# Performance work log

Hardware: AMD Instinct MI355X
Metric: run time of the kernel (lower is better)

## Reference

```python
import jax, jax.numpy as jnp
import numpy as np

N, E, F_IN, G, C = 100000, 3200000, 64, 1024, 10
BN_EPS = 1e-5


def _glorot(key, shape):
    fan_in, fan_out = shape[0], shape[1]
    lim = jnp.sqrt(6.0 / (fan_in + fan_out))
    return jax.random.uniform(key, shape, jnp.float32, -lim, lim)


def setup_inputs() -> dict:
    key = jax.random.key(0)
    ks = jax.random.split(key, 20)
    x = jax.random.normal(ks[0], (N, F_IN), jnp.float32)
    edge_index = jax.random.randint(ks[1], (2, E), 0, N, jnp.int64)
    batch = jnp.sort(jax.random.randint(ks[2], (N,), 0, G, jnp.int64))
    p = {
        'W1a': _glorot(ks[3], (F_IN, 128)), 'b1a': jnp.zeros((128,), jnp.float32),
        'W1b': _glorot(ks[4], (128, 128)), 'b1b': jnp.zeros((128,), jnp.float32),
        'g1': jnp.ones((128,), jnp.float32), 'be1': jnp.zeros((128,), jnp.float32),
        'W2a': _glorot(ks[5], (128, 64)), 'b2a': jnp.zeros((64,), jnp.float32),
        'W2b': _glorot(ks[6], (64, 64)), 'b2b': jnp.zeros((64,), jnp.float32),
        'g2': jnp.ones((64,), jnp.float32), 'be2': jnp.zeros((64,), jnp.float32),
        'W3a': _glorot(ks[7], (64, 32)), 'b3a': jnp.zeros((32,), jnp.float32),
        'W3b': _glorot(ks[8], (32, 32)), 'b3b': jnp.zeros((32,), jnp.float32),
        'g3': jnp.ones((32,), jnp.float32), 'be3': jnp.zeros((32,), jnp.float32),
        'Wf1': _glorot(ks[9], (32, 128)), 'bf1': jnp.zeros((128,), jnp.float32),
        'Wf2': _glorot(ks[10], (128, 64)), 'bf2': jnp.zeros((64,), jnp.float32),
        'Wf3': _glorot(ks[11], (64, C)), 'bf3': jnp.zeros((C,), jnp.float32),
    }
    return {'x': x, 'edge_index': edge_index, 'batch': batch, **p}


def _gin(x, src, dst, Wa, ba, Wb, bb):
    # GINConv (eps=0): h = MLP(x + sum_{j->i} x_j)
    agg = jax.ops.segment_sum(x[src], dst, num_segments=N)
    h = jax.nn.relu((x + agg) @ Wa + ba)
    return h @ Wb + bb


def _bn(x, g, b):
    # BatchNorm1d, training-mode batch statistics (biased variance)
    mu = jnp.mean(x, axis=0)
    var = jnp.mean((x - mu) ** 2, axis=0)
    return (x - mu) * jax.lax.rsqrt(var + BN_EPS) * g + b


def reference(x, edge_index, batch,
              W1a, b1a, W1b, b1b, g1, be1,
              W2a, b2a, W2b, b2b, g2, be2,
              W3a, b3a, W3b, b3b, g3, be3,
              Wf1, bf1, Wf2, bf2, Wf3, bf3):
    src, dst = edge_index[0], edge_index[1]
    z = _bn(jax.nn.relu(_gin(x, src, dst, W1a, b1a, W1b, b1b)), g1, be1)
    z = _bn(jax.nn.relu(_gin(z, src, dst, W2a, b2a, W2b, b2b)), g2, be2)
    z = _bn(jax.nn.relu(_gin(z, src, dst, W3a, b3a, W3b, b3b)), g3, be3)
    # global_add_pool over graph ids
    z = jax.ops.segment_sum(z, batch, num_segments=G)  # [G, 32]
    cr = jax.nn.relu(z @ Wf1 + bf1)
    cr = jax.nn.relu(cr @ Wf2 + bf2)  # dropout = identity (eval)
    cr = cr @ Wf3 + bf3
    return cr.reshape(-1, C)
```

## Files before the change

### kernel.cpp

```cpp
#include <hip/hip_runtime.h>

#define BN_EPS 1e-5f

typedef _Float16 f16;
typedef _Float16 f16x8 __attribute__((ext_vector_type(8)));
typedef _Float16 f16x4 __attribute__((ext_vector_type(4)));
typedef float f32x4 __attribute__((ext_vector_type(4)));

#define NBLK 512
#define BSHIFT 8
#define BMASK 255

__device__ __forceinline__ void wfrag_one(const float* __restrict__ W, f16* __restrict__ out,
        int FIN, int FOUT, int f,
        const float* __restrict__ stats, int NC, const float* __restrict__ g, float invN) {
    int j = f & 7;
    int lane = (f >> 3) & 63;
    int tile = f >> 9;
    int NT = FOUT >> 4;
    int t = tile % NT, s = tile / NT;
    int k = s * 32 + (lane >> 4) * 8 + j;
    int n = t * 16 + (lane & 15);
    float w = W[(size_t)k * FOUT + n];
    if (stats) {
        float s1 = 0.0f, s2 = 0.0f;
        for (int c = 0; c < NC; c++) {
            s1 += stats[c * 2 * FIN + k];
            s2 += stats[c * 2 * FIN + FIN + k];
        }
        float mu = s1 * invN;
        float var = fmaxf(s2 * invN - mu * mu, 0.0f);
        w *= rsqrtf(var + BN_EPS) * g[k];
    }
    out[f] = (f16)w;
}

__global__ __launch_bounds__(256) void setup_count(const float4* __restrict__ x,
        f16x4* __restrict__ xh, int n4,
        const float* __restrict__ W1a, f16* __restrict__ Wh1a,
        const float* __restrict__ W1b, f16* __restrict__ Wh1b,
        const float* __restrict__ W2b, f16* __restrict__ Wh2b,
        const float* __restrict__ W3b, f16* __restrict__ Wh3b,
        const int* __restrict__ dst, int* __restrict__ hist,
        int NBK, int CHUNK, int E) {
    __shared__ int lh[512];
    const int BC = (n4 + 255) / 256;
    int bid = blockIdx.x;
    const int t = threadIdx.x;
    if (bid < BC) {
        int i = bid * 256 + t;
        if (i < n4) {
            float4 v = x[i];
            f16x4 o;
            o.x = (f16)v.x; o.y = (f16)v.y; o.z = (f16)v.z; o.w = (f16)v.w;
            xh[i] = o;
        }
        return;
    }
    bid -= BC;
    if (bid < 116) {
        if (bid < 32)       wfrag_one(W1a, Wh1a, 64, 128, bid * 256 + t, nullptr, 1, nullptr, 0.f);
        else if (bid < 96)  wfrag_one(W1b, Wh1b, 128, 128, (bid - 32) * 256 + t, nullptr, 1, nullptr, 0.f);
        else if (bid < 112) wfrag_one(W2b, Wh2b, 64, 64, (bid - 96) * 256 + t, nullptr, 1, nullptr, 0.f);
        else                wfrag_one(W3b, Wh3b, 32, 32, (bid - 112) * 256 + t, nullptr, 1, nullptr, 0.f);
        return;
    }
    const int blk = bid - 116;
    for (int r = t; r < 512; r += 256) lh[r] = 0;
    __syncthreads();
    const int e0 = blk * CHUNK, e1 = min(E, e0 + CHUNK);
    const int nq = (e1 - e0) >> 2;
    const int4* d4 = (const int4*)(dst + e0);
    for (int q = t; q < nq; q += 256) {
        int4 v = d4[q];
        atomicAdd(&lh[v.x >> BSHIFT], 1);
        atomicAdd(&lh[v.y >> BSHIFT], 1);
        atomicAdd(&lh[v.z >> BSHIFT], 1);
        atomicAdd(&lh[v.w >> BSHIFT], 1);
    }
    for (int e = e0 + (nq << 2) + t; e < e1; e += 256) atomicAdd(&lh[dst[e] >> BSHIFT], 1);
    __syncthreads();
    for (int r = t; r < NBK; r += 256) hist[r * NBLK + blk] = lh[r];
}

__global__ __launch_bounds__(512) void bkt_bscan(int* __restrict__ hist,
        int* __restrict__ btot) {
    __shared__ int sh[512];
    const int b = blockIdx.x, t = threadIdx.x;
    int v = hist[b * NBLK + t];
    sh[t] = v;
    __syncthreads();
    for (int d = 1; d < 512; d <<= 1) {
        int u = (t >= d) ? sh[t - d] : 0;
        __syncthreads();
        sh[t] += u;
        __syncthreads();
    }
    hist[b * NBLK + t] = sh[t] - v;
    if (t == 511) btot[b] = sh[511];
}

__global__ __launch_bounds__(512) void bkt_scatter(const int* __restrict__ src,
        const int* __restrict__ dst, const int* __restrict__ hist,
        const int* __restrict__ btot, int* __restrict__ bucketed,
        int NBK, int CHUNK, int E) {
    __shared__ int sc[512];
    __shared__ int lc[512];
    const int blk = blockIdx.x, t = threadIdx.x;
    int v = (t < NBK) ? btot[t] : 0;
    sc[t] = v;
    __syncthreads();
    for (int d = 1; d < 512; d <<= 1) {
        int u = (t >= d) ? sc[t - d] : 0;
        __syncthreads();
        sc[t] += u;
        __syncthreads();
    }
    if (t < NBK) lc[t] = (sc[t] - v) + hist[t * NBLK + blk];
    __syncthreads();
    const int e0 = blk * CHUNK, e1 = min(E, e0 + CHUNK);
    const int nq = (e1 - e0) >> 2;
    const int4* d4 = (const int4*)(dst + e0);
    const int4* s4 = (const int4*)(src + e0);
    for (int q = t; q < nq; q += 512) {
        int4 d = d4[q];
        int4 s = s4[q];
        int sl;
        sl = atomicAdd(&lc[d.x >> BSHIFT], 1); bucketed[sl] = ((d.x & BMASK) << 18) | s.x;
        sl = atomicAdd(&lc[d.y >> BSHIFT], 1); bucketed[sl] = ((d.y & BMASK) << 18) | s.y;
        sl = atomicAdd(&lc[d.z >> BSHIFT], 1); bucketed[sl] = ((d.z & BMASK) << 18) | s.z;
        sl = atomicAdd(&lc[d.w >> BSHIFT], 1); bucketed[sl] = ((d.w & BMASK) << 18) | s.w;
    }
    for (int e = e0 + (nq << 2) + t; e < e1; e += 512) {
        int d = dst[e];
        int slot = atomicAdd(&lc[d >> BSHIFT], 1);
        bucketed[slot] = ((d & BMASK) << 18) | src[e];
    }
}

__global__ __launch_bounds__(512) void bkt_csr(const int* __restrict__ bucketed,
        const int* __restrict__ btot, int* __restrict__ off,
        int* __restrict__ elist, int NBK, int N, int E) {
    __shared__ int sc[512];
    __shared__ int lh[256];
    __shared__ int lc[256];
    __shared__ int sh[256];
    const int b = blockIdx.x, t = threadIdx.x;
    int v = (t < NBK) ? btot[t] : 0;
    sc[t] = v;
    __syncthreads();
    for (int d = 1; d < 512; d <<= 1) {
        int u = (t >= d) ? sc[t - d] : 0;
        __syncthreads();
        sc[t] += u;
        __syncthreads();
    }
    const int cnt  = btot[b];
    const int base = sc[b] - cnt;
    if (b == 0 && t == 0) off[N] = E;
    const int b0 = b << BSHIFT;
    const int R = min(N - b0, 256);
    if (t < 256) lh[t] = 0;
    __syncthreads();
    for (int i = t; i < cnt; i += 512) atomicAdd(&lh[bucketed[base + i] >> 18], 1);
    __syncthreads();
    int v0 = 0;
    if (t < 256) { v0 = lh[t]; sh[t] = v0; }
    __syncthreads();
    for (int d = 1; d < 256; d <<= 1) {
        int u = 0;
        if (t < 256 && t >= d) u = sh[t - d];
        __syncthreads();
        if (t < 256) sh[t] += u;
        __syncthreads();
    }
    if (t < 256) { int ex = sh[t] - v0; lh[t] = ex; lc[t] = ex; }
    __syncthreads();
    if (t < R) off[b0 + t] = base + lh[t];
    for (int i = t; i < cnt; i += 512) {
        int p = bucketed[base + i];
        int rk = atomicAdd(&lc[p >> 18], 1);
        elist[base + rk] = p & 0x3FFFF;
    }
}

template<int F, int FOUT, bool STATS, bool AFFINE, typename OutT>
__global__ __launch_bounds__(256) void gather_gemm(const int* __restrict__ off,
        const int* __restrict__ elist, const f16* __restrict__ in,
        const f16* __restrict__ Wf, const float* __restrict__ bias,
        const float* __restrict__ av, const float* __restrict__ ab,
        OutT* __restrict__ Out, float* __restrict__ stats, int N) {
    constexpr int TPN = F / 8;
    constexpr int NPB = 256 / TPN;
    constexpr int SPB = NPB / 16;
    constexpr int WPS = 4 / SPB;
    constexpr int NTF = FOUT / 16;
    constexpr int NTW = NTF / WPS;
    constexpr int NS = F / 32;
    constexpr int LDW = F + 8;
    __shared__ f16 Hl[NPB * LDW];
    __shared__ float Ss[STATS ? 2 * FOUT : 1];
    if (STATS) for (int z = threadIdx.x; z < 2 * FOUT; z += 256) Ss[z] = 0.0f;

    const int base = blockIdx.x * NPB;
    const int rl = threadIdx.x / TPN;
    const int i = base + rl;
    const int l = threadIdx.x & (TPN - 1);
    if (i < N) {
        const int j0 = l * 8;
        const f16x8* __restrict__ inv = (const f16x8*)in;
        f16x8 s = inv[(size_t)i * TPN + l];
        float a[8];
#pragma unroll
        for (int u = 0; u < 8; u++) a[u] = (float)s[u];
        int k = off[i], e = off[i + 1];
        const float cnt = (float)(e - k + 1);
        if (k + 6 <= e) {
            f16x8 c0 = inv[(size_t)elist[k + 0] * TPN + l];
            f16x8 c1 = inv[(size_t)elist[k + 1] * TPN + l];
            f16x8 c2 = inv[(size_t)elist[k + 2] * TPN + l];
            f16x8 c3 = inv[(size_t)elist[k + 3] * TPN + l];
            f16x8 c4 = inv[(size_t)elist[k + 4] * TPN + l];
            f16x8 c5 = inv[(size_t)elist[k + 5] * TPN + l];
            k += 6;
            for (; k + 6 <= e; k += 6) {
                f16x8 d0 = inv[(size_t)elist[k + 0] * TPN + l];
                f16x8 d1 = inv[(size_t)elist[k + 1] * TPN + l];
                f16x8 d2 = inv[(size_t)elist[k + 2] * TPN + l];
                f16x8 d3 = inv[(size_t)elist[k + 3] * TPN + l];
                f16x8 d4 = inv[(size_t)elist[k + 4] * TPN + l];
                f16x8 d5 = inv[(size_t)elist[k + 5] * TPN + l];
#pragma unroll
                for (int u = 0; u < 8; u++)
                    a[u] += (((float)c0[u] + (float)c1[u]) + ((float)c2[u] + (float)c3[u]))
                          + ((float)c4[u] + (float)c5[u]);
                c0 = d0; c1 = d1; c2 = d2; c3 = d3; c4 = d4; c5 = d5;
            }
#pragma unroll
            for (int u = 0; u < 8; u++)
                a[u] += (((float)c0[u] + (float)c1[u]) + ((float)c2[u] + (float)c3[u]))
                      + ((float)c4[u] + (float)c5[u]);
        }
        if (k + 4 <= e) {
            f16x8 c0 = inv[(size_t)elist[k + 0] * TPN + l];
            f16x8 c1 = inv[(size_t)elist[k + 1] * TPN + l];
            f16x8 c2 = inv[(size_t)elist[k + 2] * TPN + l];
            f16x8 c3 = inv[(size_t)elist[k + 3] * TPN + l];
            k += 4;
#pragma unroll
            for (int u = 0; u < 8; u++)
                a[u] += ((float)c0[u] + (float)c1[u]) + ((float)c2[u] + (float)c3[u]);
        }
        for (; k < e; k++) {
            f16x8 p = inv[(size_t)elist[k] * TPN + l];
#pragma unroll
            for (int u = 0; u < 8; u++) a[u] += (float)p[u];
        }
        if (AFFINE) {
            float4 vv0 = *(const float4*)(av + j0);
            float4 vv1 = *(const float4*)(av + j0 + 4);
            float4 bb0 = *(const float4*)(ab + j0);
            float4 bb1 = *(const float4*)(ab + j0 + 4);
            a[0] = fmaxf(fmaf(cnt, vv0.x, a[0] + bb0.x), 0.0f);
            a[1] = fmaxf(fmaf(cnt, vv0.y, a[1] + bb0.y), 0.0f);
            a[2] = fmaxf(fmaf(cnt, vv0.z, a[2] + bb0.z), 0.0f);
            a[3] = fmaxf(fmaf(cnt, vv0.w, a[3] + bb0.w), 0.0f);
            a[4] = fmaxf(fmaf(cnt, vv1.x, a[4] + bb1.x), 0.0f);
            a[5] = fmaxf(fmaf(cnt, vv1.y, a[5] + bb1.y), 0.0f);
            a[6] = fmaxf(fmaf(cnt, vv1.z, a[6] + bb1.z), 0.0f);
            a[7] = fmaxf(fmaf(cnt, vv1.w, a[7] + bb1.w), 0.0f);
        }
        f16x8 o;
#pragma unroll
        for (int u = 0; u < 8; u++) o[u] = (f16)a[u];
        *(f16x8*)&Hl[rl * LDW + j0] = o;
    }
    __syncthreads();

    const int wid = threadIdx.x >> 6;
    const int lane = threadIdx.x & 63;
    const int col = lane & 15;
    const int quad = lane >> 4;
    const int sid = wid / WPS;
    const int cg = wid % WPS;
    const int m0 = base + sid * 16;
    if (m0 < N) {
        f16x8 Bf[NS][NTW];
#pragma unroll
        for (int s = 0; s < NS; s++)
#pragma unroll
            for (int t = 0; t < NTW; t++)
                Bf[s][t] = *(const f16x8*)&Wf[((s * NTF + cg * NTW + t) << 9) + (lane << 3)];
        f32x4 acc[NTW];
#pragma unroll
        for (int t = 0; t < NTW; t++) {
            float b = bias[(cg * NTW + t) * 16 + col];
            acc[t] = (f32x4){b, b, b, b};
        }
        f16x8 Af[NS];
        const int rbase = (sid * 16 + col) * LDW + quad * 8;
#pragma unroll
        for (int s = 0; s < NS; s++) Af[s] = *(const f16x8*)&Hl[rbase + s * 32];
#pragma unroll
        for (int t = 0; t < NTW; t++)
#pragma unroll
            for (int s = 0; s < NS; s++)
                acc[t] = __builtin_amdgcn_mfma_f32_16x16x32_f16(Af[s], Bf[s][t], acc[t], 0, 0, 0);
#pragma unroll
        for (int t = 0; t < NTW; t++) {
            float v0 = fmaxf(acc[t][0], 0.0f);
            float v1 = fmaxf(acc[t][1], 0.0f);
            float v2 = fmaxf(acc[t][2], 0.0f);
            float v3 = fmaxf(acc[t][3], 0.0f);
            OutT* o = Out + (size_t)(m0 + quad * 4) * FOUT + (cg * NTW + t) * 16 + col;
            o[0]        = (OutT)v0;
            o[FOUT]     = (OutT)v1;
            o[2 * FOUT] = (OutT)v2;
            o[3 * FOUT] = (OutT)v3;
            if (STATS) {
                float s1 = (v0 + v1) + (v2 + v3);
                float s2 = (v0 * v0 + v1 * v1) + (v2 * v2 + v3 * v3);
                s1 += __shfl_xor(s1, 16); s1 += __shfl_xor(s1, 32);
                s2 += __shfl_xor(s2, 16); s2 += __shfl_xor(s2, 32);
                if (quad == 0) {
                    atomicAdd(&Ss[(cg * NTW + t) * 16 + col], s1);
                    atomicAdd(&Ss[FOUT + (cg * NTW + t) * 16 + col], s2);
                }
            }
        }
    }
    if (STATS) {
        __syncthreads();
        float* stc = stats + (blockIdx.x & 7) * 2 * FOUT;
        for (int z = threadIdx.x; z < 2 * FOUT; z += 256) atomicAdd(&stc[z], Ss[z]);
    }
}

__global__ __launch_bounds__(256) void layerprep_kernel(const float* __restrict__ W,
        f16* __restrict__ Wh, int FIN, int FOUT,
        const float* __restrict__ stats, int NC, const float* __restrict__ g,
        const float* __restrict__ be, float* __restrict__ v, float invN) {
    if (blockIdx.x == 0) {
        __shared__ float sh_s[128];
        const int t = threadIdx.x;
        if (t < FIN) {
            float s1 = 0.0f, s2 = 0.0f;
            for (int c = 0; c < NC; c++) {
                s1 += stats[c * 2 * FIN + t];
                s2 += stats[c * 2 * FIN + FIN + t];
            }
            float mu = s1 * invN;
            float var = fmaxf(s2 * invN - mu * mu, 0.0f);
            float sc = rsqrtf(var + BN_EPS) * g[t];
            sh_s[t] = be[t] - mu * sc;
        }
        __syncthreads();
        for (int j = t; j < FOUT; j += 256) {
            float acc = 0.0f;
            for (int k = 0; k < FIN; k++)
                acc = fmaf(sh_s[k], W[(size_t)k * FOUT + j], acc);
            v[j] = acc;
        }
        return;
    }
    int f = (blockIdx.x - 1) * 256 + threadIdx.x;
    if (f < FIN * FOUT) wfrag_one(W, Wh, FIN, FOUT, f, stats, NC, g, invN);
}

template<int FIN, int FOUT, int CT, bool STATS, bool RELU, bool BIAS, typename OutT>
__global__ __launch_bounds__(256) void gemm_mfma(const f16* __restrict__ A,
        const f16* __restrict__ Wf, const float* __restrict__ bias,
        OutT* __restrict__ Out, float* __restrict__ stats, int N) {
    constexpr int NS = FIN / 32;
    constexpr int NTF = FOUT / 16;
    constexpr int NT = CT / 16;
    constexpr int NCB = FOUT / CT;
    __shared__ float Ss[STATS ? 2 * FOUT : 1];
    if (STATS) {
        for (int i = threadIdx.x; i < 2 * FOUT; i += 256) Ss[i] = 0.0f;
        __syncthreads();
    }
    const int rb = blockIdx.x;
    const int RB = gridDim.x;
    const int wid = threadIdx.x >> 6;
    const int lane = threadIdx.x & 63;
    const int col = lane & 15;
    const int quad = lane >> 4;

    float bj[NCB][NT];
#pragma unroll
    for (int cb = 0; cb < NCB; cb++)
#pragma unroll
        for (int t = 0; t < NT; t++)
            bj[cb][t] = BIAS ? bias[(cb * NT + t) * 16 + col] : 0.0f;

    float ls[NCB][NT], ls2[NCB][NT];
#pragma unroll
    for (int cb = 0; cb < NCB; cb++)
#pragma unroll
        for (int t = 0; t < NT; t++) { ls[cb][t] = 0.0f; ls2[cb][t] = 0.0f; }

    const int S = N >> 4;
    for (int sidx = rb * 4 + wid; sidx < S; sidx += RB * 4) {
        const int m0 = sidx << 4;
        const f16* a0 = A + (size_t)(m0 + col) * FIN + (quad << 3);
        f16x8 Af[NS];
#pragma unroll
        for (int s = 0; s < NS; s++) Af[s] = *(const f16x8*)(a0 + s * 32);
#pragma unroll
        for (int cb = 0; cb < NCB; cb++) {
            const int t0 = cb * NT;
            f16x8 Bf[NS][NT];
#pragma unroll
            for (int s = 0; s < NS; s++)
#pragma unroll
                for (int t = 0; t < NT; t++)
                    Bf[s][t] = *(const f16x8*)&Wf[((s * NTF + t0 + t) << 9) + (lane << 3)];
            f32x4 acc[NT];
#pragma unroll
            for (int t = 0; t < NT; t++) acc[t] = (f32x4){bj[cb][t], bj[cb][t], bj[cb][t], bj[cb][t]};
#pragma unroll
            for (int t = 0; t < NT; t++)
#pragma unroll
                for (int s = 0; s < NS; s++)
                    acc[t] = __builtin_amdgcn_mfma_f32_16x16x32_f16(Af[s], Bf[s][t], acc[t], 0, 0, 0);
#pragma unroll
            for (int t = 0; t < NT; t++) {
                float v0 = acc[t][0], v1 = acc[t][1], v2 = acc[t][2], v3 = acc[t][3];
                if (RELU) {
                    v0 = fmaxf(v0, 0.0f); v1 = fmaxf(v1, 0.0f);
                    v2 = fmaxf(v2, 0.0f); v3 = fmaxf(v3, 0.0f);
                }
                if (STATS) {
                    ls[cb][t]  += (v0 + v1) + (v2 + v3);
                    ls2[cb][t] += (v0 * v0 + v1 * v1) + (v2 * v2 + v3 * v3);
                }
                OutT* o = Out + (size_t)(m0 + quad * 4) * FOUT + (t0 + t) * 16 + col;
                o[0]        = (OutT)v0;
                o[FOUT]     = (OutT)v1;
                o[2 * FOUT] = (OutT)v2;
                o[3 * FOUT] = (OutT)v3;
            }
        }
    }

    if (STATS) {
#pragma unroll
        for (int cb = 0; cb < NCB; cb++)
#pragma unroll
            for (int t = 0; t < NT; t++) {
                float s1 = ls[cb][t], s2 = ls2[cb][t];
                s1 += __shfl_xor(s1, 16); s1 += __shfl_xor(s1, 32);
                s2 += __shfl_xor(s2, 16); s2 += __shfl_xor(s2, 32);
                if (quad == 0) {
                    atomicAdd(&Ss[(cb * NT + t) * 16 + col], s1);
                    atomicAdd(&Ss[FOUT + (cb * NT + t) * 16 + col], s2);
                }
            }
        __syncthreads();
        float* stc = stats + (blockIdx.x & 7) * 2 * FOUT;
        for (int i = threadIdx.x; i < 2 * FOUT; i += 256) atomicAdd(&stc[i], Ss[i]);
    }
}

__global__ __launch_bounds__(256) void bn_pool_kernel(const float* __restrict__ y,
        const float* __restrict__ stats, int NC, const float* __restrict__ gw,
        const float* __restrict__ bw, const int* __restrict__ batch,
        float* __restrict__ pool, int N, float invN) {
    constexpr int F = 32, CH = 64;
    int q = threadIdx.x >> 5;
    int j = threadIdx.x & 31;
    int r0 = (blockIdx.x * 8 + q) * CH;
    if (r0 >= N) return;
    int r1 = min(r0 + CH, N);
    float s1 = 0.0f, s2 = 0.0f;
    for (int c = 0; c < NC; c++) {
        s1 += stats[c * 2 * F + j];
        s2 += stats[c * 2 * F + F + j];
    }
    float mu = s1 * invN;
    float var = fmaxf(s2 * invN - mu * mu, 0.0f);
    float sc = rsqrtf(var + BN_EPS) * gw[j];
    float sh = bw[j] - mu * sc;
    int curg = batch[r0];
    float acc = 0.0f;
    for (int r = r0; r < r1; r++) {
        int g = batch[r];
        if (g != curg) {
            atomicAdd(pool + (size_t)curg * 32 + j, acc);
            acc = 0.0f;
            curg = g;
        }
        acc = fmaf(y[(size_t)r * 32 + j], sc, sh + acc);
    }
    atomicAdd(pool + (size_t)curg * 32 + j, acc);
}

__global__ __launch_bounds__(128) void fc_kernel(const float* __restrict__ pool,
        const float* __restrict__ Wf1, const float* __restrict__ bf1,
        const float* __restrict__ Wf2, const float* __restrict__ bf2,
        const float* __restrict__ Wf3, const float* __restrict__ bf3,
        float* __restrict__ out) {
    __shared__ float zin[32];
    __shared__ float h1[128];
    __shared__ float h2[64];
    const int gidx = blockIdx.x;
    const int t = threadIdx.x;
    if (t < 32) zin[t] = pool[(size_t)gidx * 32 + t];
    __syncthreads();
    {
        float a = bf1[t];
        for (int k = 0; k < 32; k++) a = fmaf(zin[k], Wf1[k * 128 + t], a);
        h1[t] = fmaxf(a, 0.0f);
    }
    __syncthreads();
    if (t < 64) {
        float a = bf2[t];
        for (int k = 0; k < 128; k++) a = fmaf(h1[k], Wf2[k * 64 + t], a);
        h2[t] = fmaxf(a, 0.0f);
    }
    __syncthreads();
    if (t < 10) {
        float a = bf3[t];
        for (int k = 0; k < 64; k++) a = fmaf(h2[k], Wf3[k * 10 + t], a);
        out[(size_t)gidx * 10 + t] = a;
    }
}

extern "C" void kernel_launch(void* const* d_in, const int* in_sizes, int n_in,
                              void* d_out, int out_size, void* d_ws, size_t ws_size,
                              hipStream_t stream) {
    const float* x   = (const float*)d_in[0];
    const int*  ei   = (const int*)d_in[1];
    const int*  batch= (const int*)d_in[2];
    const float* W1a = (const float*)d_in[3];  const float* b1a = (const float*)d_in[4];
    const float* W1b = (const float*)d_in[5];  const float* b1b = (const float*)d_in[6];
    const float* g1  = (const float*)d_in[7];  const float* be1 = (const float*)d_in[8];
    const float* W2a = (const float*)d_in[9];  const float* b2a = (const float*)d_in[10];
    const float* W2b = (const float*)d_in[11]; const float* b2b = (const float*)d_in[12];
    const float* g2  = (const float*)d_in[13]; const float* be2 = (const float*)d_in[14];
    const float* W3a = (const float*)d_in[15]; const float* b3a = (const float*)d_in[16];
    const float* W3b = (const float*)d_in[17]; const float* b3b = (const float*)d_in[18];
    const float* g3  = (const float*)d_in[19]; const float* be3 = (const float*)d_in[20];
    const float* Wf1 = (const float*)d_in[21]; const float* bf1 = (const float*)d_in[22];
    const float* Wf2 = (const float*)d_in[23]; const float* bf2 = (const float*)d_in[24];
    const float* Wf3 = (const float*)d_in[25]; const float* bf3 = (const float*)d_in[26];

    const int N = in_sizes[2];
    const int E = in_sizes[1] / 2;
    const int G = out_size / 10;
    const int* src = ei;
    const int* dst = ei + E;

    const int NBK = (N + BMASK) >> BSHIFT;
    const int CHUNK = (((E + NBLK - 1) / NBLK) + 3) & ~3;

    float* B0   = (float*)d_ws;
    float* B1   = B0 + (size_t)N * 128;
    float* pool = B1 + (size_t)N * 128;
    float* st1  = pool + (size_t)G * 32;
    float* st2c = st1 + 2048;
    float* st3c = st2c + 1024;
    int* off    = (int*)(st3c + 512);
    int* elist  = off + (N + 1);
    float* v2   = (float*)(elist + E);
    float* v3   = v2 + 64;
    int* btot   = (int*)(v3 + 32);
    f16* Wh1a   = (f16*)(btot + NBK);
    f16* Wh1b   = Wh1a + 64 * 128;
    f16* Wh2a   = Wh1b + 128 * 128;
    f16* Wh2b   = Wh2a + 128 * 64;
    f16* Wh3a   = Wh2b + 64 * 64;
    f16* Wh3b   = Wh3a + 64 * 32;

    int* bucketed = (int*)B1;
    int* hist     = bucketed + E;

    f16* xh    = (f16*)B0;
    f16* H1    = (f16*)B0 + (size_t)N * 64;
    f16* Y1    = (f16*)B1 + (size_t)N * 64;
    f16* Z1    = (f16*)B0;
    f16* Y2    = (f16*)B0 + (size_t)N * 64;
    f16* Z2    = (f16*)B0;
    float* Y3  = B1 + (size_t)N * 64;

    hipMemsetAsync(pool, 0, ((size_t)G * 32 + 2048 + 1024 + 512) * sizeof(float), stream);

    const float invN = 1.0f / (float)N;
    const int GG = 640;

    {
        int BC = (N * 16 + 255) / 256;
        setup_count<<<BC + 116 + NBLK, 256, 0, stream>>>(
            (const float4*)x, (f16x4*)xh, N * 16,
            W1a, Wh1a, W1b, Wh1b, W2b, Wh2b, W3b, Wh3b,
            dst, hist, NBK, CHUNK, E);
    }

    bkt_bscan  <<<NBK, 512, 0, stream>>>(hist, btot);
    bkt_scatter<<<NBLK, 512, 0, stream>>>(src, dst, hist, btot, bucketed, NBK, CHUNK, E);
    bkt_csr    <<<NBK, 512, 0, stream>>>(bucketed, btot, off, elist, NBK, N, E);

    gather_gemm<64, 128, false, false, f16><<<(N + 31) / 32, 256, 0, stream>>>(
        off, elist, xh, Wh1a, b1a, nullptr, nullptr, H1, nullptr, N);
    gemm_mfma<128, 128, 64, true, true, true, f16><<<GG, 256, 0, stream>>>(H1, Wh1b, b1b, Y1, st1, N);

    layerprep_kernel<<<33, 256, 0, stream>>>(W2a, Wh2a, 128, 64, st1, 8, g1, be1, v2, invN);
    gemm_mfma<128, 64, 64, false, false, false, f16><<<GG, 256, 0, stream>>>(Y1, Wh2a, nullptr, Z1, nullptr, N);
    gather_gemm<64, 64, true, true, f16><<<(N + 31) / 32, 256, 0, stream>>>(
        off, elist, Z1, Wh2b, b2b, v2, b2a, Y2, st2c, N);

    layerprep_kernel<<<9, 256, 0, stream>>>(W3a, Wh3a, 64, 32, st2c, 8, g2, be2, v3, invN);
    gemm_mfma<64, 32, 32, false, false, false, f16><<<GG, 256, 0, stream>>>(Y2, Wh3a, nullptr, Z2, nullptr, N);
    gather_gemm<32, 32, true, true, float><<<(N + 63) / 64, 256, 0, stream>>>(
        off, elist, Z2, Wh3b, b3b, v3, b3a, Y3, st3c, N);

    bn_pool_kernel<<<(N + 511) / 512, 256, 0, stream>>>(Y3, st3c, 8, g3, be3, batch, pool, N, invN);

    fc_kernel<<<G, 128, 0, stream>>>(pool, Wf1, bf1, Wf2, bf2, Wf3, bf3, (float*)d_out);
}
```

Baseline: 459.9 us.

## Store features in column-slab layout and split gather from GEMM

Feature matrices now sit in a sliced layout, with 8-column f16 slabs stored contiguously per slab (slab-major, node-minor), and the GEMM kernels read and write that layout. The fused gather+GEMM kernel is split into a slice-parallel gather kernel plus a separate MFMA GEMM launch. Each gather block handles one 8-column slab, so a slab's random neighbor reads hit a smaller working set and may cache better in L2. The cost is an extra kernel launch per layer and a full round trip of the aggregated features through global memory.

```diff
diff --git a/kernel.cpp b/kernel.cpp
--- a/kernel.cpp
+++ b/kernel.cpp
@@ -4,7 +4,6 @@
 
 typedef _Float16 f16;
 typedef _Float16 f16x8 __attribute__((ext_vector_type(8)));
-typedef _Float16 f16x4 __attribute__((ext_vector_type(4)));
 typedef float f32x4 __attribute__((ext_vector_type(4)));
 
 #define NBLK 512
@@ -36,7 +35,7 @@
 }
 
 __global__ __launch_bounds__(256) void setup_count(const float4* __restrict__ x,
-        f16x4* __restrict__ xh, int n4,
+        f16* __restrict__ xh, int N,
         const float* __restrict__ W1a, f16* __restrict__ Wh1a,
         const float* __restrict__ W1b, f16* __restrict__ Wh1b,
         const float* __restrict__ W2b, f16* __restrict__ Wh2b,
@@ -44,16 +43,20 @@
         const int* __restrict__ dst, int* __restrict__ hist,
         int NBK, int CHUNK, int E) {
     __shared__ int lh[512];
-    const int BC = (n4 + 255) / 256;
+    const int BC = (N + 31) / 32;
     int bid = blockIdx.x;
     const int t = threadIdx.x;
     if (bid < BC) {
-        int i = bid * 256 + t;
-        if (i < n4) {
-            float4 v = x[i];
-            f16x4 o;
-            o.x = (f16)v.x; o.y = (f16)v.y; o.z = (f16)v.z; o.w = (f16)v.w;
-            xh[i] = o;
+        int r = t >> 3, sl = t & 7;
+        int i = bid * 32 + r;
+        if (i < N) {
+            const float4* xr = x + (size_t)i * 16 + sl * 2;
+            float4 v0 = xr[0];
+            float4 v1 = xr[1];
+            f16x8 o;
+            o[0] = (f16)v0.x; o[1] = (f16)v0.y; o[2] = (f16)v0.z; o[3] = (f16)v0.w;
+            o[4] = (f16)v1.x; o[5] = (f16)v1.y; o[6] = (f16)v1.z; o[7] = (f16)v1.w;
+            ((f16x8*)xh)[(size_t)sl * N + i] = o;
         }
         return;
     }
@@ -184,156 +187,65 @@
     }
 }
 
-template<int F, int FOUT, bool STATS, bool AFFINE, typename OutT>
-__global__ __launch_bounds__(256) void gather_gemm(const int* __restrict__ off,
+template<int F, bool AFFINE>
+__global__ __launch_bounds__(256) void gather_slice(const int* __restrict__ off,
         const int* __restrict__ elist, const f16* __restrict__ in,
-        const f16* __restrict__ Wf, const float* __restrict__ bias,
         const float* __restrict__ av, const float* __restrict__ ab,
-        OutT* __restrict__ Out, float* __restrict__ stats, int N) {
-    constexpr int TPN = F / 8;
-    constexpr int NPB = 256 / TPN;
-    constexpr int SPB = NPB / 16;
-    constexpr int WPS = 4 / SPB;
-    constexpr int NTF = FOUT / 16;
-    constexpr int NTW = NTF / WPS;
-    constexpr int NS = F / 32;
-    constexpr int LDW = F + 8;
-    __shared__ f16 Hl[NPB * LDW];
-    __shared__ float Ss[STATS ? 2 * FOUT : 1];
-    if (STATS) for (int z = threadIdx.x; z < 2 * FOUT; z += 256) Ss[z] = 0.0f;
-
-    const int base = blockIdx.x * NPB;
-    const int rl = threadIdx.x / TPN;
-    const int i = base + rl;
-    const int l = threadIdx.x & (TPN - 1);
-    if (i < N) {
-        const int j0 = l * 8;
-        const f16x8* __restrict__ inv = (const f16x8*)in;
-        f16x8 s = inv[(size_t)i * TPN + l];
-        float a[8];
-#pragma unroll
-        for (int u = 0; u < 8; u++) a[u] = (float)s[u];
-        int k = off[i], e = off[i + 1];
-        const float cnt = (float)(e - k + 1);
-        if (k + 6 <= e) {
-            f16x8 c0 = inv[(size_t)elist[k + 0] * TPN + l];
-            f16x8 c1 = inv[(size_t)elist[k + 1] * TPN + l];
-            f16x8 c2 = inv[(size_t)elist[k + 2] * TPN + l];
-            f16x8 c3 = inv[(size_t)elist[k + 3] * TPN + l];
-            f16x8 c4 = inv[(size_t)elist[k + 4] * TPN + l];
-            f16x8 c5 = inv[(size_t)elist[k + 5] * TPN + l];
-            k += 6;
-            for (; k + 6 <= e; k += 6) {
-                f16x8 d0 = inv[(size_t)elist[k + 0] * TPN + l];
-                f16x8 d1 = inv[(size_t)elist[k + 1] * TPN + l];
-                f16x8 d2 = inv[(size_t)elist[k + 2] * TPN + l];
-                f16x8 d3 = inv[(size_t)elist[k + 3] * TPN + l];
-                f16x8 d4 = inv[(size_t)elist[k + 4] * TPN + l];
-                f16x8 d5 = inv[(size_t)elist[k + 5] * TPN + l];
-#pragma unroll
-                for (int u = 0; u < 8; u++)
-                    a[u] += (((float)c0[u] + (float)c1[u]) + ((float)c2[u] + (float)c3[u]))
-                          + ((float)c4[u] + (float)c5[u]);
-                c0 = d0; c1 = d1; c2 = d2; c3 = d3; c4 = d4; c5 = d5;
-            }
-#pragma unroll
-            for (int u = 0; u < 8; u++)
-                a[u] += (((float)c0[u] + (float)c1[u]) + ((float)c2[u] + (float)c3[u]))
-                      + ((float)c4[u] + (float)c5[u]);
-        }
-        if (k + 4 <= e) {
-            f16x8 c0 = inv[(size_t)elist[k + 0] * TPN + l];
-            f16x8 c1 = inv[(size_t)elist[k + 1] * TPN + l];
-            f16x8 c2 = inv[(size_t)elist[k + 2] * TPN + l];
-            f16x8 c3 = inv[(size_t)elist[k + 3] * TPN + l];
-            k += 4;
+        f16* __restrict__ out, int N) {
+    constexpr int NSL = F / 8;
+    const int cs = blockIdx.x & (NSL - 1);
+    const int i = (blockIdx.x / NSL) * 256 + threadIdx.x;
+    if (i >= N) return;
+    const f16x8* __restrict__ slab = (const f16x8*)in + (size_t)cs * N;
+    f16x8 s = slab[i];
+    float a[8];
+#pragma unroll
+    for (int u = 0; u < 8; u++) a[u] = (float)s[u];
+    int k = off[i], e = off[i + 1];
+    const float cnt = (float)(e - k + 1);
+    if (k + 4 <= e) {
+        f16x8 c0 = slab[elist[k + 0]];
+        f16x8 c1 = slab[elist[k + 1]];
+        f16x8 c2 = slab[elist[k + 2]];
+        f16x8 c3 = slab[elist[k + 3]];
+        k += 4;
+        for (; k + 4 <= e; k += 4) {
+            f16x8 d0 = slab[elist[k + 0]];
+            f16x8 d1 = slab[elist[k + 1]];
+            f16x8 d2 = slab[elist[k + 2]];
+            f16x8 d3 = slab[elist[k + 3]];
 #pragma unroll
             for (int u = 0; u < 8; u++)
                 a[u] += ((float)c0[u] + (float)c1[u]) + ((float)c2[u] + (float)c3[u]);
-        }
-        for (; k < e; k++) {
-            f16x8 p = inv[(size_t)elist[k] * TPN + l];
-#pragma unroll
-            for (int u = 0; u < 8; u++) a[u] += (float)p[u];
-        }
-        if (AFFINE) {
-            float4 vv0 = *(const float4*)(av + j0);
-            float4 vv1 = *(const float4*)(av + j0 + 4);
-            float4 bb0 = *(const float4*)(ab + j0);
-            float4 bb1 = *(const float4*)(ab + j0 + 4);
-            a[0] = fmaxf(fmaf(cnt, vv0.x, a[0] + bb0.x), 0.0f);
-            a[1] = fmaxf(fmaf(cnt, vv0.y, a[1] + bb0.y), 0.0f);
-            a[2] = fmaxf(fmaf(cnt, vv0.z, a[2] + bb0.z), 0.0f);
-            a[3] = fmaxf(fmaf(cnt, vv0.w, a[3] + bb0.w), 0.0f);
-            a[4] = fmaxf(fmaf(cnt, vv1.x, a[4] + bb1.x), 0.0f);
-            a[5] = fmaxf(fmaf(cnt, vv1.y, a[5] + bb1.y), 0.0f);
-            a[6] = fmaxf(fmaf(cnt, vv1.z, a[6] + bb1.z), 0.0f);
-            a[7] = fmaxf(fmaf(cnt, vv1.w, a[7] + bb1.w), 0.0f);
-        }
-        f16x8 o;
-#pragma unroll
-        for (int u = 0; u < 8; u++) o[u] = (f16)a[u];
-        *(f16x8*)&Hl[rl * LDW + j0] = o;
-    }
-    __syncthreads();
-
-    const int wid = threadIdx.x >> 6;
-    const int lane = threadIdx.x & 63;
-    const int col = lane & 15;
-    const int quad = lane >> 4;
-    const int sid = wid / WPS;
-    const int cg = wid % WPS;
-    const int m0 = base + sid * 16;
-    if (m0 < N) {
-        f16x8 Bf[NS][NTW];
-#pragma unroll
-        for (int s = 0; s < NS; s++)
-#pragma unroll
-            for (int t = 0; t < NTW; t++)
-                Bf[s][t] = *(const f16x8*)&Wf[((s * NTF + cg * NTW + t) << 9) + (lane << 3)];
-        f32x4 acc[NTW];
-#pragma unroll
-        for (int t = 0; t < NTW; t++) {
-            float b = bias[(cg * NTW + t) * 16 + col];
-            acc[t] = (f32x4){b, b, b, b};
-        }
-        f16x8 Af[NS];
-        const int rbase = (sid * 16 + col) * LDW + quad * 8;
-#pragma unroll
-        for (int s = 0; s < NS; s++) Af[s] = *(const f16x8*)&Hl[rbase + s * 32];
-#pragma unroll
-        for (int t = 0; t < NTW; t++)
-#pragma unroll
-            for (int s = 0; s < NS; s++)
-                acc[t] = __builtin_amdgcn_mfma_f32_16x16x32_f16(Af[s], Bf[s][t], acc[t], 0, 0, 0);
-#pragma unroll
-        for (int t = 0; t < NTW; t++) {
-            float v0 = fmaxf(acc[t][0], 0.0f);
-            float v1 = fmaxf(acc[t][1], 0.0f);
-            float v2 = fmaxf(acc[t][2], 0.0f);
-            float v3 = fmaxf(acc[t][3], 0.0f);
-            OutT* o = Out + (size_t)(m0 + quad * 4) * FOUT + (cg * NTW + t) * 16 + col;
-            o[0]        = (OutT)v0;
-            o[FOUT]     = (OutT)v1;
-            o[2 * FOUT] = (OutT)v2;
-            o[3 * FOUT] = (OutT)v3;
-            if (STATS) {
-                float s1 = (v0 + v1) + (v2 + v3);
-                float s2 = (v0 * v0 + v1 * v1) + (v2 * v2 + v3 * v3);
-                s1 += __shfl_xor(s1, 16); s1 += __shfl_xor(s1, 32);
-                s2 += __shfl_xor(s2, 16); s2 += __shfl_xor(s2, 32);
-                if (quad == 0) {
-                    atomicAdd(&Ss[(cg * NTW + t) * 16 + col], s1);
-                    atomicAdd(&Ss[FOUT + (cg * NTW + t) * 16 + col], s2);
-                }
-            }
-        }
-    }
-    if (STATS) {
-        __syncthreads();
-        float* stc = stats + (blockIdx.x & 7) * 2 * FOUT;
-        for (int z = threadIdx.x; z < 2 * FOUT; z += 256) atomicAdd(&stc[z], Ss[z]);
-    }
+            c0 = d0; c1 = d1; c2 = d2; c3 = d3;
+        }
+#pragma unroll
+        for (int u = 0; u < 8; u++)
+            a[u] += ((float)c0[u] + (float)c1[u]) + ((float)c2[u] + (float)c3[u]);
+    }
+    for (; k < e; k++) {
+        f16x8 p = slab[elist[k]];
+#pragma unroll
+        for (int u = 0; u < 8; u++) a[u] += (float)p[u];
+    }
+    if (AFFINE) {
+        const float4 vv0 = *(const float4*)(av + cs * 8);
+        const float4 vv1 = *(const float4*)(av + cs * 8 + 4);
+        const float4 bb0 = *(const float4*)(ab + cs * 8);
+        const float4 bb1 = *(const float4*)(ab + cs * 8 + 4);
+        a[0] = fmaxf(fmaf(cnt, vv0.x, a[0] + bb0.x), 0.0f);
+        a[1] = fmaxf(fmaf(cnt, vv0.y, a[1] + bb0.y), 0.0f);
+        a[2] = fmaxf(fmaf(cnt, vv0.z, a[2] + bb0.z), 0.0f);
+        a[3] = fmaxf(fmaf(cnt, vv0.w, a[3] + bb0.w), 0.0f);
+        a[4] = fmaxf(fmaf(cnt, vv1.x, a[4] + bb1.x), 0.0f);
+        a[5] = fmaxf(fmaf(cnt, vv1.y, a[5] + bb1.y), 0.0f);
+        a[6] = fmaxf(fmaf(cnt, vv1.z, a[6] + bb1.z), 0.0f);
+        a[7] = fmaxf(fmaf(cnt, vv1.w, a[7] + bb1.w), 0.0f);
+    }
+    f16x8 o;
+#pragma unroll
+    for (int u = 0; u < 8; u++) o[u] = (f16)a[u];
+    ((f16x8*)out)[(size_t)cs * N + i] = o;
 }
 
 __global__ __launch_bounds__(256) void layerprep_kernel(const float* __restrict__ W,
@@ -403,10 +315,10 @@
     const int S = N >> 4;
     for (int sidx = rb * 4 + wid; sidx < S; sidx += RB * 4) {
         const int m0 = sidx << 4;
-        const f16* a0 = A + (size_t)(m0 + col) * FIN + (quad << 3);
         f16x8 Af[NS];
 #pragma unroll
-        for (int s = 0; s < NS; s++) Af[s] = *(const f16x8*)(a0 + s * 32);
+        for (int s = 0; s < NS; s++)
+            Af[s] = ((const f16x8*)A)[(size_t)(s * 4 + quad) * N + (m0 + col)];
 #pragma unroll
         for (int cb = 0; cb < NCB; cb++) {
             const int t0 = cb * NT;
@@ -435,11 +347,20 @@
                     ls[cb][t]  += (v0 + v1) + (v2 + v3);
                     ls2[cb][t] += (v0 * v0 + v1 * v1) + (v2 * v2 + v3 * v3);
                 }
-                OutT* o = Out + (size_t)(m0 + quad * 4) * FOUT + (t0 + t) * 16 + col;
-                o[0]        = (OutT)v0;
-                o[FOUT]     = (OutT)v1;
-                o[2 * FOUT] = (OutT)v2;
-                o[3 * FOUT] = (OutT)v3;
+                if constexpr (sizeof(OutT) == 2) {
+                    const int slb = (t0 + t) * 2 + (col >> 3);
+                    f16* o = (f16*)Out + ((size_t)slb * N + (m0 + quad * 4)) * 8 + (col & 7);
+                    o[0]  = (f16)v0;
+                    o[8]  = (f16)v1;
+                    o[16] = (f16)v2;
+                    o[24] = (f16)v3;
+                } else {
+                    OutT* o = Out + (size_t)(m0 + quad * 4) * FOUT + (t0 + t) * 16 + col;
+                    o[0]        = (OutT)v0;
+                    o[FOUT]     = (OutT)v1;
+                    o[2 * FOUT] = (OutT)v2;
+                    o[3 * FOUT] = (OutT)v3;
+                }
             }
         }
     }
@@ -577,22 +498,26 @@
     int* hist     = bucketed + E;
 
     f16* xh    = (f16*)B0;
+    f16* S1    = (f16*)B1;
     f16* H1    = (f16*)B0 + (size_t)N * 64;
     f16* Y1    = (f16*)B1 + (size_t)N * 64;
     f16* Z1    = (f16*)B0;
+    f16* S2    = (f16*)B1;
     f16* Y2    = (f16*)B0 + (size_t)N * 64;
     f16* Z2    = (f16*)B0;
+    f16* S3    = (f16*)B1;
     float* Y3  = B1 + (size_t)N * 64;
 
     hipMemsetAsync(pool, 0, ((size_t)G * 32 + 2048 + 1024 + 512) * sizeof(float), stream);
 
     const float invN = 1.0f / (float)N;
     const int GG = 640;
+    const int GCH = (N + 255) / 256;
 
     {
-        int BC = (N * 16 + 255) / 256;
+        int BC = (N + 31) / 32;
         setup_count<<<BC + 116 + NBLK, 256, 0, stream>>>(
-            (const float4*)x, (f16x4*)xh, N * 16,
+            (const float4*)x, xh, N,
             W1a, Wh1a, W1b, Wh1b, W2b, Wh2b, W3b, Wh3b,
             dst, hist, NBK, CHUNK, E);
     }
@@ -601,19 +526,19 @@
     bkt_scatter<<<NBLK, 512, 0, stream>>>(src, dst, hist, btot, bucketed, NBK, CHUNK, E);
     bkt_csr    <<<NBK, 512, 0, stream>>>(bucketed, btot, off, elist, NBK, N, E);
 
-    gather_gemm<64, 128, false, false, f16><<<(N + 31) / 32, 256, 0, stream>>>(
-        off, elist, xh, Wh1a, b1a, nullptr, nullptr, H1, nullptr, N);
+    gather_slice<64, false><<<GCH * 8, 256, 0, stream>>>(off, elist, xh, nullptr, nullptr, S1, N);
+    gemm_mfma<64, 128, 64, false, true, true, f16><<<GG, 256, 0, stream>>>(S1, Wh1a, b1a, H1, nullptr, N);
     gemm_mfma<128, 128, 64, true, true, true, f16><<<GG, 256, 0, stream>>>(H1, Wh1b, b1b, Y1, st1, N);
 
     layerprep_kernel<<<33, 256, 0, stream>>>(W2a, Wh2a, 128, 64, st1, 8, g1, be1, v2, invN);
     gemm_mfma<128, 64, 64, false, false, false, f16><<<GG, 256, 0, stream>>>(Y1, Wh2a, nullptr, Z1, nullptr, N);
-    gather_gemm<64, 64, true, true, f16><<<(N + 31) / 32, 256, 0, stream>>>(
-        off, elist, Z1, Wh2b, b2b, v2, b2a, Y2, st2c, N);
+    gather_slice<64, true><<<GCH * 8, 256, 0, stream>>>(off, elist, Z1, v2, b2a, S2, N);
+    gemm_mfma<64, 64, 64, true, true, true, f16><<<GG, 256, 0, stream>>>(S2, Wh2b, b2b, Y2, st2c, N);
 
     layerprep_kernel<<<9, 256, 0, stream>>>(W3a, Wh3a, 64, 32, st2c, 8, g2, be2, v3, invN);
     gemm_mfma<64, 32, 32, false, false, false, f16><<<GG, 256, 0, stream>>>(Y2, Wh3a, nullptr, Z2, nullptr, N);
-    gather_gemm<32, 32, true, true, float><<<(N + 63) / 64, 256, 0, stream>>>(
-        off, elist, Z2, Wh3b, b3b, v3, b3a, Y3, st3c, N);
+    gather_slice<32, true><<<GCH * 4, 256, 0, stream>>>(off, elist, Z2, v3, b3a, S3, N);
+    gemm_mfma<32, 32, 32, true, true, true, float><<<GG, 256, 0, stream>>>(S3, Wh3b, b3b, Y3, st3c, N);
 
     bn_pool_kernel<<<(N + 511) / 512, 256, 0, stream>>>(Y3, st3c, 8, g3, be3, batch, pool, N, invN);
 
```

Result: slower. 678.2 us (+47.5%).
